# Kernel optimization log

Hardware: AMD Instinct MI355X
Metric: run time of the kernel (lower is better)

## Reference

```python
import jax, jax.numpy as jnp
import numpy as np

D_MODEL = 1024
NHEAD = 16
D_K = D_MODEL // NHEAD


def setup_inputs() -> dict:
    key = jax.random.key(0)
    ks = jax.random.split(key, 11)
    B, S = 2, 2048
    scale = 1.0 / np.sqrt(D_MODEL)
    inp = {
        "q": jax.random.normal(ks[0], (B, S, D_MODEL), jnp.float32),
        "k": jax.random.normal(ks[1], (B, S, D_MODEL), jnp.float32),
        "v": jax.random.normal(ks[2], (B, S, D_MODEL), jnp.float32),
        "Wq": jax.random.normal(ks[3], (D_MODEL, D_MODEL), jnp.float32) * scale,
        "bq": jnp.zeros((D_MODEL,), jnp.float32),
        "Wk": jax.random.normal(ks[4], (D_MODEL, D_MODEL), jnp.float32) * scale,
        "bk": jnp.zeros((D_MODEL,), jnp.float32),
        "Wv": jax.random.normal(ks[5], (D_MODEL, D_MODEL), jnp.float32) * scale,
        "bv": jnp.zeros((D_MODEL,), jnp.float32),
        "Wo": jax.random.normal(ks[6], (D_MODEL, D_MODEL), jnp.float32) * scale,
        "bo": jnp.zeros((D_MODEL,), jnp.float32),
    }
    return inp


def reference(q, k, v, Wq, bq, Wk, bk, Wv, bv, Wo, bo):
    B, S, _ = q.shape
    # Linear projections (torch Linear: x @ W.T + b), split into heads
    def proj(x, W, b):
        y = jnp.einsum('bsd,ed->bse', x, W) + b
        return y.reshape(B, -1, NHEAD, D_K).transpose(0, 2, 1, 3)  # [B,H,S,Dk]

    qh = proj(q, Wq, bq)
    kh = proj(k, Wk, bk)
    vh = proj(v, Wv, bv)

    scores = jnp.einsum('bhqd,bhkd->bhqk', qh, kh) / jnp.sqrt(
        jnp.asarray(D_K, qh.dtype))
    attn = jax.nn.softmax(scores, axis=-1)  # dropout is identity in eval
    out = jnp.einsum('bhqk,bhkd->bhqd', attn, vh)
    out = out.transpose(0, 2, 1, 3).reshape(B, S, D_MODEL)
    return jnp.einsum('bsd,ed->bse', out, Wo) + bo
```

## Files before the change

kernel.cpp:

```cpp
#include <hip/hip_runtime.h>
#include <stdint.h>
#include <stddef.h>

#define D_MODEL 1024
#define NHEAD   16
#define DK      64
#define BB      2
#define SS      2048
#define NTOK    (BB*SS)

#define SCALE_Q 0.18033688011f

typedef short  short8 __attribute__((ext_vector_type(8)));
typedef __bf16 bf16x8 __attribute__((ext_vector_type(8)));
typedef float  f32x4  __attribute__((ext_vector_type(4)));

__device__ __forceinline__ unsigned short f2bf(float x){
  unsigned int u = __builtin_bit_cast(unsigned int, x);
  u += 0x7fffu + ((u >> 16) & 1u);
  return (unsigned short)(u >> 16);
}

__device__ __forceinline__ unsigned int pack_bf2(float x, float y){
  unsigned int a = __builtin_bit_cast(unsigned int, x) + 0x8000u;
  unsigned int b = __builtin_bit_cast(unsigned int, y) + 0x8000u;
  return __builtin_amdgcn_perm(b, a, 0x07060302u);
}

__device__ __forceinline__ float fast_exp2(float x){
#if __has_builtin(__builtin_amdgcn_exp2f)
  return __builtin_amdgcn_exp2f(x);
#else
  return exp2f(x);
#endif
}

__device__ __forceinline__ f32x4 mfma16(bf16x8 a, bf16x8 b, f32x4 c){
  return __builtin_amdgcn_mfma_f32_16x16x32_bf16(a, b, c, 0, 0, 0);
}

__device__ __forceinline__ void async16(const void* g, void* lds){
  __builtin_amdgcn_global_load_lds(
      (const __attribute__((address_space(1))) unsigned int*)g,
      (__attribute__((address_space(3))) unsigned int*)lds,
      16, 0, 0);
}

__global__ __launch_bounds__(256) void cast_bf16_all(
    const float* __restrict__ q,  const float* __restrict__ k,  const float* __restrict__ v,
    const float* __restrict__ wq, const float* __restrict__ wk, const float* __restrict__ wv,
    const float* __restrict__ wo,
    unsigned short* __restrict__ qb,  unsigned short* __restrict__ kb,  unsigned short* __restrict__ vb,
    unsigned short* __restrict__ wqb, unsigned short* __restrict__ wkb, unsigned short* __restrict__ wvb,
    unsigned short* __restrict__ wob)
{
  const float* src; unsigned short* dst; int n;
  switch (blockIdx.y){
    case 0: src = q;  dst = qb;  n = NTOK*D_MODEL;    break;
    case 1: src = k;  dst = kb;  n = NTOK*D_MODEL;    break;
    case 2: src = v;  dst = vb;  n = NTOK*D_MODEL;    break;
    case 3: src = wq; dst = wqb; n = D_MODEL*D_MODEL; break;
    case 4: src = wk; dst = wkb; n = D_MODEL*D_MODEL; break;
    case 5: src = wv; dst = wvb; n = D_MODEL*D_MODEL; break;
    default: src = wo; dst = wob; n = D_MODEL*D_MODEL; break;
  }
  int i = (blockIdx.x * 256 + threadIdx.x) * 8;
  if (i >= n) return;
  float4 a = *(const float4*)(src + i);
  float4 b = *(const float4*)(src + i + 4);
  short8 o;
  o[0] = (short)f2bf(a.x); o[1] = (short)f2bf(a.y);
  o[2] = (short)f2bf(a.z); o[3] = (short)f2bf(a.w);
  o[4] = (short)f2bf(b.x); o[5] = (short)f2bf(b.y);
  o[6] = (short)f2bf(b.z); o[7] = (short)f2bf(b.w);
  *(short8*)(dst + i) = o;
}

__global__ __launch_bounds__(256) void qkv_gemm(
    const unsigned short* __restrict__ qb, const unsigned short* __restrict__ kb,
    const unsigned short* __restrict__ vb,
    const unsigned short* __restrict__ wqb, const unsigned short* __restrict__ wkb,
    const unsigned short* __restrict__ wvb,
    const float* __restrict__ bq, const float* __restrict__ bk, const float* __restrict__ bv,
    unsigned short* __restrict__ Qh, unsigned short* __restrict__ Kh, unsigned short* __restrict__ Vt)
{
  __shared__ __align__(16) unsigned short As[128*64];
  __shared__ __align__(16) unsigned short Bs[128*64];
  const int id = blockIdx.x, z = id >> 8, r = id & 255;
  const unsigned short *A, *Bt; const float* bias; unsigned short* C;
  int bm, bn, N, brow; float scale;
  if (z == 0){ A = qb;  Bt = wqb; bias = bq; C = Qh; bm = (r>>3)*128; bn = (r&7)*128; N = 1024; brow = 0; scale = SCALE_Q; }
  else if (z == 1){ A = kb;  Bt = wkb; bias = bk; C = Kh; bm = (r>>3)*128; bn = (r&7)*128; N = 1024; brow = 0; scale = 1.0f; }
  else            { A = wvb; Bt = vb;  bias = bv; C = Vt; bm = (r&7)*128; bn = (r>>3)*128; N = 4096; brow = 1; scale = 1.0f; }
  const int K = 1024;
  const int tid  = threadIdx.x, lane = tid & 63, w = tid >> 6;
  const int quad = lane >> 4,   l16  = lane & 15;
  const int wm = w >> 1, wn = w & 1;
  const int sw = l16 & 7;
  f32x4 acc[4][4] = {};
  for (int kb_ = 0; kb_ < 16; ++kb_){
    const int k0 = kb_ << 6;
    __syncthreads();
    #pragma unroll
    for (int c = 0; c < 4; ++c){
      int chunk = (w*4 + c)*64 + lane;
      int row = chunk >> 3, c8 = chunk & 7;
      int cs = (c8 ^ (row & 7)) << 3;
      async16(A  + (size_t)(bm + row)*K + k0 + cs, (char*)As + (w*4 + c)*1024);
      async16(Bt + (size_t)(bn + row)*K + k0 + cs, (char*)Bs + (w*4 + c)*1024);
    }
    __syncthreads();
    bf16x8 af[4][2], bf[4][2];
    #pragma unroll
    for (int mt = 0; mt < 4; ++mt)
      #pragma unroll
      for (int ks = 0; ks < 2; ++ks){
        int off = (((ks*4 + quad) ^ sw) << 3);
        af[mt][ks] = *(const bf16x8*)&As[(wm*64 + mt*16 + l16)*64 + off];
        bf[mt][ks] = *(const bf16x8*)&Bs[(wn*64 + mt*16 + l16)*64 + off];
      }
    #pragma unroll
    for (int ks = 0; ks < 2; ++ks)
      #pragma unroll
      for (int mt = 0; mt < 4; ++mt)
        #pragma unroll
        for (int nt = 0; nt < 4; ++nt)
          acc[mt][nt] = mfma16(af[mt][ks], bf[nt][ks], acc[mt][nt]);
  }
  const int m0 = bm + wm*64, n0 = bn + wn*64;
  #pragma unroll
  for (int mt = 0; mt < 4; ++mt){
    #pragma unroll
    for (int nt = 0; nt < 4; ++nt){
      int col = n0 + nt*16 + l16;
      float bc = brow ? 0.0f : bias[col];
      #pragma unroll
      for (int rr = 0; rr < 4; ++rr){
        int row = m0 + mt*16 + quad*4 + rr;
        float val = (acc[mt][nt][rr] + (brow ? bias[row] : bc)) * scale;
        C[(size_t)row*N + col] = f2bf(val);
      }
    }
  }
}

__global__ __launch_bounds__(256) void gemm_out(
    const unsigned short* __restrict__ A, const unsigned short* __restrict__ Bt,
    const float* __restrict__ bias, float* __restrict__ C)
{
  __shared__ __align__(16) unsigned short As[64*64];
  __shared__ __align__(16) unsigned short Bs[128*64];
  const int K = 1024, N = 1024;
  const int tid  = threadIdx.x, lane = tid & 63, w = tid >> 6;
  const int quad = lane >> 4,   l16  = lane & 15;
  const int bm = blockIdx.y * 64, bn = blockIdx.x * 128;
  const int sw = l16 & 7;
  f32x4 acc[4][2] = {};
  for (int kb_ = 0; kb_ < 16; ++kb_){
    const int k0 = kb_ << 6;
    __syncthreads();
    #pragma unroll
    for (int c = 0; c < 2; ++c){
      int chunk = (w*2 + c)*64 + lane;
      int row = chunk >> 3, c8 = chunk & 7;
      async16(A + (size_t)(bm + row)*K + k0 + ((c8 ^ (row & 7)) << 3),
              (char*)As + (w*2 + c)*1024);
    }
    #pragma unroll
    for (int c = 0; c < 4; ++c){
      int chunk = (w*4 + c)*64 + lane;
      int row = chunk >> 3, c8 = chunk & 7;
      async16(Bt + (size_t)(bn + row)*K + k0 + ((c8 ^ (row & 7)) << 3),
              (char*)Bs + (w*4 + c)*1024);
    }
    __syncthreads();
    bf16x8 af[4][2], bf[2][2];
    #pragma unroll
    for (int mt = 0; mt < 4; ++mt)
      #pragma unroll
      for (int ks = 0; ks < 2; ++ks)
        af[mt][ks] = *(const bf16x8*)&As[(mt*16 + l16)*64 + (((ks*4 + quad) ^ sw) << 3)];
    #pragma unroll
    for (int nt = 0; nt < 2; ++nt)
      #pragma unroll
      for (int ks = 0; ks < 2; ++ks)
        bf[nt][ks] = *(const bf16x8*)&Bs[(w*32 + nt*16 + l16)*64 + (((ks*4 + quad) ^ sw) << 3)];
    #pragma unroll
    for (int ks = 0; ks < 2; ++ks)
      #pragma unroll
      for (int mt = 0; mt < 4; ++mt)
        #pragma unroll
        for (int nt = 0; nt < 2; ++nt)
          acc[mt][nt] = mfma16(af[mt][ks], bf[nt][ks], acc[mt][nt]);
  }
  #pragma unroll
  for (int mt = 0; mt < 4; ++mt){
    #pragma unroll
    for (int nt = 0; nt < 2; ++nt){
      int col = bn + w*32 + nt*16 + l16;
      float bc = bias[col];
      #pragma unroll
      for (int rr = 0; rr < 4; ++rr){
        int row = bm + mt*16 + quad*4 + rr;
        C[(size_t)row*N + col] = acc[mt][nt][rr] + bc;
      }
    }
  }
}

__global__ __launch_bounds__(256) void attn(
    const unsigned short* __restrict__ Qh, const unsigned short* __restrict__ Kh,
    const unsigned short* __restrict__ Vt, unsigned short* __restrict__ ctx)
{
  __shared__ __align__(16) unsigned short Kbuf[2][64*64];
  __shared__ __align__(16) unsigned short Vbuf[2][64*64];
  __shared__ __align__(16) unsigned short QP[128*64];

  const int tid  = threadIdx.x, lane = tid & 63, w = tid >> 6;
  const int quad = lane >> 4,   l16  = lane & 15;
  const int b = blockIdx.y >> 4, h = blockIdx.y & 15;
  const int q0 = blockIdx.x * 128;
  const int sw = l16 & 7;

  #pragma unroll
  for (int c = 0; c < 4; ++c){
    int s = (w*4 + c)*64 + lane;
    int row = s >> 3, c8 = s & 7;
    async16(Qh + (size_t)(b*SS + q0 + row)*D_MODEL + h*DK + ((c8 ^ (row & 7)) << 3),
            (char*)QP + (w*4 + c)*1024);
  }

  const unsigned short* Kp = Kh + (size_t)(b*SS)*D_MODEL + h*DK;
  const unsigned short* Vp = Vt + (size_t)(h*DK)*NTOK + b*SS;
  const unsigned short* ksrc[2];
  const unsigned short* vsrc[2];
  #pragma unroll
  for (int c = 0; c < 2; ++c){
    int s = (w*2 + c)*64 + lane;
    int row = s >> 3, c8 = s & 7;
    int cs = (c8 ^ (row & 7)) << 3;
    ksrc[c] = Kp + (size_t)row*D_MODEL + cs;
    vsrc[c] = Vp + (size_t)row*NTOK  + cs;
  }

  #pragma unroll
  for (int c = 0; c < 2; ++c){
    async16(ksrc[c], (char*)Kbuf[0] + (w*2 + c)*1024);
    async16(vsrc[c], (char*)Vbuf[0] + (w*2 + c)*1024);
    ksrc[c] += 64*D_MODEL;
    vsrc[c] += 64;
  }
  __syncthreads();

  bf16x8 bq0[2], bq1[2];
  #pragma unroll
  for (int ks = 0; ks < 2; ++ks){
    bq0[ks] = *(const bf16x8*)&QP[(w*32 +      l16)*64 + (((ks*4 + quad) ^ sw) << 3)];
    bq1[ks] = *(const bf16x8*)&QP[(w*32 + 16 + l16)*64 + (((ks*4 + quad) ^ sw) << 3)];
  }

  f32x4 acc[2][4] = {};
  float l_i[2] = {0.0f, 0.0f};

  for (int it = 0; it < 32; ++it){
    const int cur = it & 1;
    #pragma unroll
    for (int c = 0; c < 2; ++c){
      async16(ksrc[c], (char*)Kbuf[1 - cur] + (w*2 + c)*1024);
      async16(vsrc[c], (char*)Vbuf[1 - cur] + (w*2 + c)*1024);
      ksrc[c] += 64*D_MODEL;
      vsrc[c] += 64;
    }
    asm volatile("s_waitcnt vmcnt(4)\n\ts_barrier" ::: "memory");

    const unsigned short* Kc = Kbuf[cur];
    const unsigned short* Vc = Vbuf[cur];

    bf16x8 kf[4][2];
    #pragma unroll
    for (int mt = 0; mt < 4; ++mt)
      #pragma unroll
      for (int ks = 0; ks < 2; ++ks)
        kf[mt][ks] = *(const bf16x8*)&Kc[(mt*16 + l16)*64 + (((ks*4 + quad) ^ sw) << 3)];

    f32x4 s0[4] = {}, s1[4] = {};
    #pragma unroll
    for (int mt = 0; mt < 4; ++mt)
      #pragma unroll
      for (int ks = 0; ks < 2; ++ks){
        s0[mt] = mfma16(kf[mt][ks], bq0[ks], s0[mt]);
        s1[mt] = mfma16(kf[mt][ks], bq1[ks], s1[mt]);
      }

    float ls0 = 0.0f, ls1 = 0.0f;
    #pragma unroll
    for (int mt = 0; mt < 4; ++mt)
      #pragma unroll
      for (int rr = 0; rr < 4; ++rr){
        float p0 = fast_exp2(s0[mt][rr]); s0[mt][rr] = p0; ls0 += p0;
        float p1 = fast_exp2(s1[mt][rr]); s1[mt][rr] = p1; ls1 += p1;
      }
    l_i[0] += ls0; l_i[1] += ls1;
    const int pr0 = (w*32 +      l16)*64;
    const int pr1 = (w*32 + 16 + l16)*64;
    #pragma unroll
    for (int mt = 0; mt < 4; ++mt){
      int c8  = mt*2 + (quad >> 1);
      int off = ((c8 ^ sw) << 3) + (quad & 1)*4;
      uint2 p;
      p.x = pack_bf2(s0[mt][0], s0[mt][1]);
      p.y = pack_bf2(s0[mt][2], s0[mt][3]);
      *(uint2*)&QP[pr0 + off] = p;
      p.x = pack_bf2(s1[mt][0], s1[mt][1]);
      p.y = pack_bf2(s1[mt][2], s1[mt][3]);
      *(uint2*)&QP[pr1 + off] = p;
    }
    asm volatile("s_waitcnt lgkmcnt(0)" ::: "memory");
    bf16x8 bp0[2], bp1[2];
    #pragma unroll
    for (int ks = 0; ks < 2; ++ks){
      bp0[ks] = *(const bf16x8*)&QP[pr0 + (((ks*4 + quad) ^ sw) << 3)];
      bp1[ks] = *(const bf16x8*)&QP[pr1 + (((ks*4 + quad) ^ sw) << 3)];
    }

    #pragma unroll
    for (int nt = 0; nt < 4; ++nt){
      bf16x8 vf0 = *(const bf16x8*)&Vc[(nt*16 + l16)*64 + (((0*4 + quad) ^ sw) << 3)];
      bf16x8 vf1 = *(const bf16x8*)&Vc[(nt*16 + l16)*64 + (((1*4 + quad) ^ sw) << 3)];
      acc[0][nt] = mfma16(vf0, bp0[0], acc[0][nt]);
      acc[1][nt] = mfma16(vf0, bp1[0], acc[1][nt]);
      acc[0][nt] = mfma16(vf1, bp0[1], acc[0][nt]);
      acc[1][nt] = mfma16(vf1, bp1[1], acc[1][nt]);
    }

    asm volatile("s_waitcnt lgkmcnt(0)\n\ts_barrier" ::: "memory");
  }

  float inv[2];
  #pragma unroll
  for (int qg = 0; qg < 2; ++qg){
    float t = l_i[qg];
    t += __shfl_xor(t, 16);
    t += __shfl_xor(t, 32);
    inv[qg] = 1.0f / t;
  }
  #pragma unroll
  for (int qg = 0; qg < 2; ++qg){
    int pr = (w*32 + qg*16 + l16)*64;
    #pragma unroll
    for (int nt = 0; nt < 4; ++nt){
      int c8  = nt*2 + (quad >> 1);
      int off = ((c8 ^ sw) << 3) + (quad & 1)*4;
      uint2 p;
      p.x = pack_bf2(acc[qg][nt][0]*inv[qg], acc[qg][nt][1]*inv[qg]);
      p.y = pack_bf2(acc[qg][nt][2]*inv[qg], acc[qg][nt][3]*inv[qg]);
      *(uint2*)&QP[pr + off] = p;
    }
  }
  asm volatile("s_waitcnt lgkmcnt(0)" ::: "memory");
  {
    int r  = w*32 + (lane >> 1);
    int j0 = (lane & 1)*4;
    unsigned short* dst = ctx + (size_t)(b*SS + q0 + r)*D_MODEL + h*DK;
    #pragma unroll
    for (int i = 0; i < 4; ++i){
      int j = j0 + i;
      uint4 d = *(const uint4*)&QP[r*64 + ((j ^ (r & 7)) << 3)];
      *(uint4*)(dst + j*8) = d;
    }
  }
}

extern "C" void kernel_launch(void* const* d_in, const int* in_sizes, int n_in,
                              void* d_out, int out_size, void* d_ws, size_t ws_size,
                              hipStream_t stream) {
  const float* q  = (const float*)d_in[0];
  const float* k  = (const float*)d_in[1];
  const float* v  = (const float*)d_in[2];
  const float* Wq = (const float*)d_in[3];
  const float* bq = (const float*)d_in[4];
  const float* Wk = (const float*)d_in[5];
  const float* bk = (const float*)d_in[6];
  const float* Wv = (const float*)d_in[7];
  const float* bv = (const float*)d_in[8];
  const float* Wo = (const float*)d_in[9];
  const float* bo = (const float*)d_in[10];

  char* ws = (char*)d_ws;
  const size_t TOKB = (size_t)NTOK * D_MODEL * 2;
  const size_t WB   = (size_t)D_MODEL * D_MODEL * 2;
  unsigned short* qb  = (unsigned short*)ws;             ws += TOKB;
  unsigned short* kb  = (unsigned short*)ws;             ws += TOKB;
  unsigned short* vb  = (unsigned short*)ws;             ws += TOKB;
  unsigned short* wqb = (unsigned short*)ws;             ws += WB;
  unsigned short* wkb = (unsigned short*)ws;             ws += WB;
  unsigned short* wvb = (unsigned short*)ws;             ws += WB;
  unsigned short* wob = (unsigned short*)ws;             ws += WB;
  unsigned short* Qh  = (unsigned short*)ws;             ws += TOKB;
  unsigned short* Kh  = (unsigned short*)ws;             ws += TOKB;
  unsigned short* Vt  = (unsigned short*)ws;             ws += TOKB;
  unsigned short* ctx = (unsigned short*)ws;             ws += TOKB;

  cast_bf16_all<<<dim3(2048, 7), 256, 0, stream>>>(q, k, v, Wq, Wk, Wv, Wo,
                                                   qb, kb, vb, wqb, wkb, wvb, wob);
  qkv_gemm<<<dim3(768), 256, 0, stream>>>(qb, kb, vb, wqb, wkb, wvb,
                                          bq, bk, bv, Qh, Kh, Vt);
  attn<<<dim3(SS/128, BB*NHEAD), 256, 0, stream>>>(Qh, Kh, Vt, ctx);
  gemm_out<<<dim3(8, 64), 256, 0, stream>>>(ctx, wob, bo, (float*)d_out);
}
```

Baseline: 232.6 us.

## Keep softmax probabilities in registers, permuting V fragment loads to match MFMA layout

Removes the LDS round trip for the P matrix in the attention loop. The probabilities are packed straight from the S accumulator registers with v_cvt_pk_bf16_f32, and the V fragments are loaded as pairs of 8-byte pieces whose k-index order matches the accumulator layout. This drops an LDS write, a waitcnt and an LDS read per tile. In exchange it adds twice as many smaller LDS reads for V, more live registers, and a changed rounding path (hardware conversion instead of add-and-truncate).

```diff
diff --git a/kernel.cpp b/kernel.cpp
--- a/kernel.cpp
+++ b/kernel.cpp
@@ -25,6 +25,12 @@
   unsigned int a = __builtin_bit_cast(unsigned int, x) + 0x8000u;
   unsigned int b = __builtin_bit_cast(unsigned int, y) + 0x8000u;
   return __builtin_amdgcn_perm(b, a, 0x07060302u);
+}
+
+__device__ __forceinline__ unsigned int cvt_pk_bf16(float lo, float hi){
+  unsigned int r;
+  asm("v_cvt_pk_bf16_f32 %0, %1, %2" : "=v"(r) : "v"(lo), "v"(hi));
+  return r;
 }
 
 __device__ __forceinline__ float fast_exp2(float x){
@@ -221,6 +227,7 @@
   const int b = blockIdx.y >> 4, h = blockIdx.y & 15;
   const int q0 = blockIdx.x * 128;
   const int sw = l16 & 7;
+  const int qh = quad >> 1, ql = (quad & 1) * 4;
 
   #pragma unroll
   for (int c = 0; c < 4; ++c){
@@ -283,6 +290,16 @@
       for (int ks = 0; ks < 2; ++ks)
         kf[mt][ks] = *(const bf16x8*)&Kc[(mt*16 + l16)*64 + (((ks*4 + quad) ^ sw) << 3)];
 
+    uint2 vfr[4][2][2];
+    #pragma unroll
+    for (int nt = 0; nt < 4; ++nt)
+      #pragma unroll
+      for (int ks = 0; ks < 2; ++ks){
+        int rb = (nt*16 + l16)*64 + ql;
+        vfr[nt][ks][0] = *(const uint2*)&Vc[rb + (((ks*4     + qh) ^ sw) << 3)];
+        vfr[nt][ks][1] = *(const uint2*)&Vc[rb + (((ks*4 + 2 + qh) ^ sw) << 3)];
+      }
+
     f32x4 s0[4] = {}, s1[4] = {};
     #pragma unroll
     for (int mt = 0; mt < 4; ++mt)
@@ -301,37 +318,34 @@
         float p1 = fast_exp2(s1[mt][rr]); s1[mt][rr] = p1; ls1 += p1;
       }
     l_i[0] += ls0; l_i[1] += ls1;
-    const int pr0 = (w*32 +      l16)*64;
-    const int pr1 = (w*32 + 16 + l16)*64;
-    #pragma unroll
-    for (int mt = 0; mt < 4; ++mt){
-      int c8  = mt*2 + (quad >> 1);
-      int off = ((c8 ^ sw) << 3) + (quad & 1)*4;
-      uint2 p;
-      p.x = pack_bf2(s0[mt][0], s0[mt][1]);
-      p.y = pack_bf2(s0[mt][2], s0[mt][3]);
-      *(uint2*)&QP[pr0 + off] = p;
-      p.x = pack_bf2(s1[mt][0], s1[mt][1]);
-      p.y = pack_bf2(s1[mt][2], s1[mt][3]);
-      *(uint2*)&QP[pr1 + off] = p;
-    }
-    asm volatile("s_waitcnt lgkmcnt(0)" ::: "memory");
+
     bf16x8 bp0[2], bp1[2];
     #pragma unroll
     for (int ks = 0; ks < 2; ++ks){
-      bp0[ks] = *(const bf16x8*)&QP[pr0 + (((ks*4 + quad) ^ sw) << 3)];
-      bp1[ks] = *(const bf16x8*)&QP[pr1 + (((ks*4 + quad) ^ sw) << 3)];
-    }
-
-    #pragma unroll
-    for (int nt = 0; nt < 4; ++nt){
-      bf16x8 vf0 = *(const bf16x8*)&Vc[(nt*16 + l16)*64 + (((0*4 + quad) ^ sw) << 3)];
-      bf16x8 vf1 = *(const bf16x8*)&Vc[(nt*16 + l16)*64 + (((1*4 + quad) ^ sw) << 3)];
-      acc[0][nt] = mfma16(vf0, bp0[0], acc[0][nt]);
-      acc[1][nt] = mfma16(vf0, bp1[0], acc[1][nt]);
-      acc[0][nt] = mfma16(vf1, bp0[1], acc[0][nt]);
-      acc[1][nt] = mfma16(vf1, bp1[1], acc[1][nt]);
-    }
+      uint4 t;
+      t.x = cvt_pk_bf16(s0[2*ks  ][0], s0[2*ks  ][1]);
+      t.y = cvt_pk_bf16(s0[2*ks  ][2], s0[2*ks  ][3]);
+      t.z = cvt_pk_bf16(s0[2*ks+1][0], s0[2*ks+1][1]);
+      t.w = cvt_pk_bf16(s0[2*ks+1][2], s0[2*ks+1][3]);
+      bp0[ks] = __builtin_bit_cast(bf16x8, t);
+      t.x = cvt_pk_bf16(s1[2*ks  ][0], s1[2*ks  ][1]);
+      t.y = cvt_pk_bf16(s1[2*ks  ][2], s1[2*ks  ][3]);
+      t.z = cvt_pk_bf16(s1[2*ks+1][0], s1[2*ks+1][1]);
+      t.w = cvt_pk_bf16(s1[2*ks+1][2], s1[2*ks+1][3]);
+      bp1[ks] = __builtin_bit_cast(bf16x8, t);
+    }
+
+    #pragma unroll
+    for (int nt = 0; nt < 4; ++nt)
+      #pragma unroll
+      for (int ks = 0; ks < 2; ++ks){
+        uint4 vv;
+        vv.x = vfr[nt][ks][0].x; vv.y = vfr[nt][ks][0].y;
+        vv.z = vfr[nt][ks][1].x; vv.w = vfr[nt][ks][1].y;
+        bf16x8 vf = __builtin_bit_cast(bf16x8, vv);
+        acc[0][nt] = mfma16(vf, bp0[ks], acc[0][nt]);
+        acc[1][nt] = mfma16(vf, bp1[ks], acc[1][nt]);
+      }
 
     asm volatile("s_waitcnt lgkmcnt(0)\n\ts_barrier" ::: "memory");
   }
```

Result: slower. 239.6 us (+3.0%).
